# Kernel tuning notes

Measured on AMD Instinct MI355X. Metric: run time of the kernel, lower is better.

The kernel has to match this reference:

```python
import jax, jax.numpy as jnp
import numpy as np

D_MODEL = 1024
N_HEADS = 16
D_K = D_MODEL // N_HEADS
B, L = 4, 2048


def setup_inputs() -> dict:
    key = jax.random.key(0)
    ks = jax.random.split(key, 9)
    s = 1.0 / np.sqrt(D_MODEL)
    return {
        "x": jax.random.normal(ks[0], (B, L, D_MODEL), dtype=jnp.float32),
        "mask": jnp.ones((B, L), dtype=jnp.int32),
        "Wq": jax.random.uniform(ks[1], (D_MODEL, D_MODEL), jnp.float32, -s, s),
        "bq": jax.random.uniform(ks[2], (D_MODEL,), jnp.float32, -s, s),
        "Wk": jax.random.uniform(ks[3], (D_MODEL, D_MODEL), jnp.float32, -s, s),
        "bk": jax.random.uniform(ks[4], (D_MODEL,), jnp.float32, -s, s),
        "Wv": jax.random.uniform(ks[5], (D_MODEL, D_MODEL), jnp.float32, -s, s),
        "bv": jax.random.uniform(ks[6], (D_MODEL,), jnp.float32, -s, s),
        "Wo": jax.random.uniform(ks[7], (D_MODEL, D_MODEL), jnp.float32, -s, s),
        "bo": jax.random.uniform(ks[8], (D_MODEL,), jnp.float32, -s, s),
    }


def reference(x, mask, Wq, bq, Wk, bk, Wv, bv, Wo, bo):
    b, l, d = x.shape
    # project and split heads: [B, H, L, d_k]
    def heads(W, bias):
        return (x @ W.T + bias).reshape(b, l, N_HEADS, D_K).transpose(0, 2, 1, 3)
    Q = heads(Wq, bq)
    K = heads(Wk, bk)
    V = heads(Wv, bv)
    scores = jnp.einsum("bhqd,bhkd->bhqk", Q, K) / np.sqrt(D_K).astype(np.float32)
    # mask: [B, L] -> broadcast over heads and query dim as [B, 1, 1, L]
    scores = jnp.where(mask[:, None, None, :] == 0, jnp.float32(-1e9), scores)
    attn = jax.nn.softmax(scores, axis=-1)  # dropout=0 in eval math
    out = jnp.einsum("bhqk,bhkd->bhqd", attn, V)
    out = out.transpose(0, 2, 1, 3).reshape(b, l, d)
    return out @ Wo.T + bo
```

## Files before the change

### kernel.cpp

```cpp
#include <hip/hip_runtime.h>
#include <stdint.h>

#define DMODEL 1024
#define NHEADS 16
#define DK     64
#define BATCH  4
#define SEQ    2048
#define MROWS  (BATCH*SEQ)

typedef __bf16 bf16x8 __attribute__((ext_vector_type(8)));
typedef float  f32x4  __attribute__((ext_vector_type(4)));

#if defined(__has_builtin)
#if __has_builtin(__builtin_amdgcn_exp2f)
#define EXP2F(x) __builtin_amdgcn_exp2f(x)
#endif
#endif
#ifndef EXP2F
#define EXP2F(x) exp2f(x)
#endif

__device__ __forceinline__ unsigned short f2bf(float f) {
    unsigned int u = __builtin_bit_cast(unsigned int, f);
    u += 0x7fffu + ((u >> 16) & 1u);
    return (unsigned short)(u >> 16);
}

__device__ __forceinline__ unsigned int pack_bf16(float a, float b) {
    unsigned int ua = __builtin_bit_cast(unsigned int, a) + 0x8000u;
    unsigned int ub = __builtin_bit_cast(unsigned int, b) + 0x8000u;
    return __builtin_amdgcn_perm(ub, ua, 0x07060302u);
}

#define GLDS(gp, lp) __builtin_amdgcn_global_load_lds( \
    (const __attribute__((address_space(1))) unsigned int*)(gp), \
    (__attribute__((address_space(3))) unsigned int*)(lp), 16, 0, 0)

__global__ void cvt_kernel(const float* __restrict__ src,
                           unsigned short* __restrict__ dst, int n4) {
    int i = blockIdx.x * blockDim.x + threadIdx.x;
    if (i >= n4) return;
    const float4 v = reinterpret_cast<const float4*>(src)[i];
    ushort4 o;
    o.x = f2bf(v.x); o.y = f2bf(v.y); o.z = f2bf(v.z); o.w = f2bf(v.w);
    reinterpret_cast<ushort4*>(dst)[i] = o;
}

__global__ void cvtw_kernel(const float* __restrict__ w0, const float* __restrict__ w1,
                            const float* __restrict__ w2, const float* __restrict__ w3,
                            unsigned short* __restrict__ d0, unsigned short* __restrict__ d1,
                            unsigned short* __restrict__ d2, unsigned short* __restrict__ d3) {
    const float* s; unsigned short* d;
    switch (blockIdx.y) {
        case 0:  s = w0; d = d0; break;
        case 1:  s = w1; d = d1; break;
        case 2:  s = w2; d = d2; break;
        default: s = w3; d = d3; break;
    }
    const int i = blockIdx.x * blockDim.x + threadIdx.x;
    const float4 v = reinterpret_cast<const float4*>(s)[i];
    ushort4 o;
    o.x = f2bf(v.x); o.y = f2bf(v.y); o.z = f2bf(v.z); o.w = f2bf(v.w);
    reinterpret_cast<ushort4*>(d)[i] = o;
}

__global__ void maskbias_kernel(const int* __restrict__ m, float* __restrict__ o, int n) {
    const int i = blockIdx.x * blockDim.x + threadIdx.x;
    if (i < n) o[i] = m[i] ? 0.f : -1e30f;
}

template<int MODE>
__global__ __launch_bounds__(512, 1) void gemm256(
        const unsigned short* __restrict__ A,
        const unsigned short* __restrict__ W0,
        const unsigned short* __restrict__ W1,
        const unsigned short* __restrict__ W2,
        const float* __restrict__ b0,
        const float* __restrict__ b1,
        const float* __restrict__ b2,
        void* __restrict__ o0, void* __restrict__ o1, void* __restrict__ o2) {
    __shared__ unsigned short As[2][256 * 64];
    __shared__ unsigned short Bs[2][128 * 64];
    const int tid  = threadIdx.x;
    const int lane = tid & 63;
    const int wave = tid >> 6;
    const int quad = lane >> 4;
    const int r15  = lane & 15;
    const int wr = wave >> 1, wc = wave & 1;
    const int m0 = blockIdx.y * 256;

    int which, ncol0;
    const unsigned short* W;
    const float* bias;
    if (MODE == 0) {
        which = blockIdx.x >> 3;
        ncol0 = (blockIdx.x & 7) * 128;
        W    = which == 0 ? W0 : (which == 1 ? W1 : W2);
        bias = which == 0 ? b0 : (which == 1 ? b1 : b2);
    } else {
        which = 0; ncol0 = blockIdx.x * 128; W = W0; bias = b0;
    }

    const int srow = lane >> 3;
    const int scg  = (lane & 7) ^ srow;
    const unsigned short* Ag[4];
    const unsigned short* Wg[2];
    #pragma unroll
    for (int j = 0; j < 4; ++j)
        Ag[j] = A + (size_t)(m0 + j * 64 + wave * 8 + srow) * DMODEL + scg * 8;
    #pragma unroll
    for (int j = 0; j < 2; ++j)
        Wg[j] = W + (size_t)(ncol0 + j * 64 + wave * 8 + srow) * DMODEL + scg * 8;

    f32x4 acc[4][4] = {};

    #pragma unroll
    for (int j = 0; j < 4; ++j) GLDS(Ag[j], &As[0][(j * 64 + wave * 8) * 64]);
    #pragma unroll
    for (int j = 0; j < 2; ++j) GLDS(Wg[j], &Bs[0][(j * 64 + wave * 8) * 64]);
    __syncthreads();

    int buf = 0;
    for (int kk = 0; kk < DMODEL; kk += 64) {
        if (kk + 64 < DMODEL) {
            #pragma unroll
            for (int j = 0; j < 4; ++j)
                GLDS(Ag[j] + kk + 64, &As[buf ^ 1][(j * 64 + wave * 8) * 64]);
            #pragma unroll
            for (int j = 0; j < 2; ++j)
                GLDS(Wg[j] + kk + 64, &Bs[buf ^ 1][(j * 64 + wave * 8) * 64]);
        }
        #pragma unroll
        for (int u = 0; u < 2; ++u) {
            bf16x8 af[4], bfx[4];
            const int cs = ((u * 4 + quad) ^ (r15 & 7)) * 8;
            #pragma unroll
            for (int t = 0; t < 4; ++t) {
                af[t]  = *(const bf16x8*)&As[buf][(wr * 64 + t * 16 + r15) * 64 + cs];
                bfx[t] = *(const bf16x8*)&Bs[buf][(wc * 64 + t * 16 + r15) * 64 + cs];
            }
            #pragma unroll
            for (int mt = 0; mt < 4; ++mt)
                #pragma unroll
                for (int nt = 0; nt < 4; ++nt)
                    acc[mt][nt] = __builtin_amdgcn_mfma_f32_16x16x32_bf16(
                        af[mt], bfx[nt], acc[mt][nt], 0, 0, 0);
        }
        __syncthreads();
        buf ^= 1;
    }

    #pragma unroll
    for (int mt = 0; mt < 4; ++mt) {
        #pragma unroll
        for (int nt = 0; nt < 4; ++nt) {
            #pragma unroll
            for (int r = 0; r < 4; ++r) {
                const int row = m0 + wr * 64 + mt * 16 + quad * 4 + r;
                const int col = ncol0 + wc * 64 + nt * 16 + r15;
                float v = acc[mt][nt][r] + bias[col];
                if (MODE == 1) {
                    ((float*)o0)[(size_t)row * DMODEL + col] = v;
                } else {
                    if (which == 0) v *= 0.18033688011112042f;
                    const int b = row >> 11, l = row & (SEQ - 1);
                    const int h = col >> 6,  d = col & (DK - 1);
                    const int bh = b * NHEADS + h;
                    unsigned short* ow = (unsigned short*)(which == 0 ? o0 : (which == 1 ? o1 : o2));
                    size_t idx;
                    if (which < 2) idx = ((size_t)bh * SEQ + l) * DK + d;
                    else           idx = (size_t)bh * (SEQ * DK) + (l >> 6) * (DK * 64) + d * 64 + (l & 63);
                    ow[idx] = f2bf(v);
                }
            }
        }
    }
}

__global__ __launch_bounds__(256, 4) void flash_attn(
        const unsigned short* __restrict__ Q,
        const unsigned short* __restrict__ Km,
        const unsigned short* __restrict__ Vm,
        const float* __restrict__ mbf,
        unsigned short* __restrict__ Oa) {
    __shared__ unsigned short Ks[2][64 * 64];
    __shared__ unsigned short Vs[64 * 64];
    __shared__ unsigned short Pl[4][2][16 * 64];
    const int lane = threadIdx.x & 63;
    const int wave = threadIdx.x >> 6;
    const int quad = lane >> 4;
    const int r15  = lane & 15;

    const int id   = (blockIdx.y << 4) | blockIdx.x;
    const int xcd  = id & 7;
    const int slot = id >> 3;
    const int bh   = xcd + ((slot >> 4) << 3);
    const int qt   = slot & 15;
    const int b = bh >> 4, h = bh & (NHEADS - 1);
    const int q0 = qt * 128 + wave * 32;

    const unsigned short* Qb = Q  + (size_t)bh * SEQ * DK;
    const unsigned short* Kb = Km + (size_t)bh * SEQ * DK;
    const unsigned short* Vb = Vm + (size_t)bh * SEQ * DK;
    const float* mb = mbf + b * SEQ;

    const int srow = lane >> 3;
    const int soff = ((lane >> 3) * 64) + (((lane & 7) ^ srow) * 8);

    bf16x8 bq[2][2];
    #pragma unroll
    for (int qf = 0; qf < 2; ++qf)
        #pragma unroll
        for (int u = 0; u < 2; ++u)
            bq[qf][u] = *(const bf16x8*)(Qb + (q0 + qf * 16 + r15) * DK + u * 32 + quad * 8);

    float l_part[2] = {0.f, 0.f};
    f32x4 oacc[2][4] = {};

    #pragma unroll
    for (int j = 0; j < 2; ++j) {
        const int wseg = wave * 2 + j;
        GLDS(Kb + wseg * 512 + soff, &Ks[0][wseg * 512]);
        GLDS(Vb + wseg * 512 + soff, &Vs[wseg * 512]);
    }
    __syncthreads();

    #define NT (SEQ / 64)
    for (int t = 0; t < NT; ++t) {
        const int kb = t * 64;
        const int cur = t & 1;

        float4 m4v[4];
        #pragma unroll
        for (int tt = 0; tt < 4; ++tt)
            m4v[tt] = *(const float4*)(mb + kb + tt * 16 + quad * 4);

        if (t + 1 < NT) {
            const unsigned short* Kg = Kb + (kb + 64) * 64;
            #pragma unroll
            for (int j = 0; j < 2; ++j) {
                const int wseg = wave * 2 + j;
                GLDS(Kg + wseg * 512 + soff, &Ks[cur ^ 1][wseg * 512]);
            }
        }

        char* const Pb = (char*)&Pl[wave][0][0];
        #pragma unroll
        for (int tt = 0; tt < 4; ++tt) {
            const bf16x8 ak0 = *(const bf16x8*)&Ks[cur][(tt * 16 + r15) * 64 + ((quad ^ (r15 & 7)) * 8)];
            const bf16x8 ak1 = *(const bf16x8*)&Ks[cur][(tt * 16 + r15) * 64 + (((4 + quad) ^ (r15 & 7)) * 8)];
            const float4 m4 = m4v[tt];
            #pragma unroll
            for (int qf = 0; qf < 2; ++qf) {
                f32x4 z = {};
                z = __builtin_amdgcn_mfma_f32_16x16x32_bf16(ak0, bq[qf][0], z, 0, 0, 0);
                z = __builtin_amdgcn_mfma_f32_16x16x32_bf16(ak1, bq[qf][1], z, 0, 0, 0);
                const float p0 = EXP2F(z[0] + m4.x);
                const float p1 = EXP2F(z[1] + m4.y);
                const float p2 = EXP2F(z[2] + m4.z);
                const float p3 = EXP2F(z[3] + m4.w);
                l_part[qf] += (p0 + p1) + (p2 + p3);
                uint2 pw;
                pw.x = pack_bf16(p0, p1);
                pw.y = pack_bf16(p2, p3);
                const int c2 = (tt * 2 + (quad >> 1)) ^ (r15 & 7);
                *(uint2*)(Pb + qf * 2048 + r15 * 128 + c2 * 16 + (quad & 1) * 8) = pw;
            }
        }

        __syncthreads();

        __builtin_amdgcn_s_setprio(1);
        #pragma unroll
        for (int u = 0; u < 2; ++u) {
            const int cs = ((u * 4 + quad) ^ (r15 & 7)) * 8;
            bf16x8 vf[4];
            #pragma unroll
            for (int nt = 0; nt < 4; ++nt)
                vf[nt] = *(const bf16x8*)&Vs[(nt * 16 + r15) * 64 + cs];
            #pragma unroll
            for (int qf = 0; qf < 2; ++qf) {
                const bf16x8 ap = *(const bf16x8*)(Pb + qf * 2048 + r15 * 128 + cs * 2);
                #pragma unroll
                for (int nt = 0; nt < 4; ++nt)
                    oacc[qf][nt] = __builtin_amdgcn_mfma_f32_16x16x32_bf16(
                        ap, vf[nt], oacc[qf][nt], 0, 0, 0);
            }
        }
        __builtin_amdgcn_s_setprio(0);

        __syncthreads();

        if (t + 1 < NT) {
            const unsigned short* Vg = Vb + (kb + 64) * 64;
            #pragma unroll
            for (int j = 0; j < 2; ++j) {
                const int wseg = wave * 2 + j;
                GLDS(Vg + wseg * 512 + soff, &Vs[wseg * 512]);
            }
        }
    }
    #undef NT

    #pragma unroll
    for (int qf = 0; qf < 2; ++qf) {
        float l = l_part[qf];
        l += __shfl_xor(l, 16);
        l += __shfl_xor(l, 32);
        float lq[4];
        #pragma unroll
        for (int r = 0; r < 4; ++r) lq[r] = __shfl(l, quad * 4 + r, 64);
        #pragma unroll
        for (int nt = 0; nt < 4; ++nt) {
            #pragma unroll
            for (int r = 0; r < 4; ++r) {
                const int row = q0 + qf * 16 + quad * 4 + r;
                const int col = h * DK + nt * 16 + r15;
                Oa[((size_t)b * SEQ + row) * DMODEL + col] = f2bf(oacc[qf][nt][r] / lq[r]);
            }
        }
    }
}

extern "C" void kernel_launch(void* const* d_in, const int* in_sizes, int n_in,
                              void* d_out, int out_size, void* d_ws, size_t ws_size,
                              hipStream_t stream) {
    (void)in_sizes; (void)n_in; (void)out_size; (void)ws_size;
    const float* x  = (const float*)d_in[0];
    const int* mask = (const int*)d_in[1];
    const float* Wq = (const float*)d_in[2];
    const float* bq = (const float*)d_in[3];
    const float* Wk = (const float*)d_in[4];
    const float* bk = (const float*)d_in[5];
    const float* Wv = (const float*)d_in[6];
    const float* bv = (const float*)d_in[7];
    const float* Wo = (const float*)d_in[8];
    const float* bo = (const float*)d_in[9];
    float* out = (float*)d_out;

    char* ws = (char*)d_ws;
    unsigned short* xb  = (unsigned short*)(ws);
    unsigned short* wqb = (unsigned short*)(ws + 16777216);
    unsigned short* wkb = (unsigned short*)(ws + 16777216 + 1 * 2097152);
    unsigned short* wvb = (unsigned short*)(ws + 16777216 + 2 * 2097152);
    unsigned short* wob = (unsigned short*)(ws + 16777216 + 3 * 2097152);
    unsigned short* qb  = (unsigned short*)(ws + 16777216 + 4 * 2097152);
    unsigned short* kb  = qb  + (size_t)MROWS * DMODEL;
    unsigned short* vtb = kb  + (size_t)MROWS * DMODEL;
    unsigned short* ab  = vtb + (size_t)MROWS * DMODEL;
    float*          mbf = (float*)(ab + (size_t)MROWS * DMODEL);

    cvt_kernel<<<dim3(MROWS * DMODEL / 4 / 256), 256, 0, stream>>>(x, xb, MROWS * DMODEL / 4);
    cvtw_kernel<<<dim3(DMODEL * DMODEL / 4 / 256, 4), 256, 0, stream>>>(
        Wq, Wk, Wv, Wo, wqb, wkb, wvb, wob);
    maskbias_kernel<<<dim3(BATCH * SEQ / 256), 256, 0, stream>>>(mask, mbf, BATCH * SEQ);

    gemm256<0><<<dim3(24, MROWS / 256), 512, 0, stream>>>(
        xb, wqb, wkb, wvb, bq, bk, bv, qb, kb, vtb);

    flash_attn<<<dim3(16, BATCH * NHEADS), 256, 0, stream>>>(qb, kb, vtb, mbf, ab);

    gemm256<1><<<dim3(8, MROWS / 256), 512, 0, stream>>>(
        ab, wob, nullptr, nullptr, bo, nullptr, nullptr, out, nullptr, nullptr);
}
```

Before: 318.6 us.

## Triple-buffer GEMM LDS stages with split prefetch and raw barriers

Both GEMMs move from double to triple buffering of the A/W tiles in LDS. The loads for stage t+2 are issued in two halves interleaved with the two MFMA sub-steps. Full __syncthreads are replaced with raw s_barrier plus explicit vmcnt waits, and s_setprio is raised around the MFMA blocks. The aim is to hide global-to-LDS latency and cut barrier stalls, at the cost of about 1.5x the LDS (144KB) and hand-managed waitcnt counts that must stay correct.

```diff
diff --git a/kernel.cpp b/kernel.cpp
--- a/kernel.cpp
+++ b/kernel.cpp
@@ -35,6 +35,9 @@
 #define GLDS(gp, lp) __builtin_amdgcn_global_load_lds( \
     (const __attribute__((address_space(1))) unsigned int*)(gp), \
     (__attribute__((address_space(3))) unsigned int*)(lp), 16, 0, 0)
+
+#define RAW_BARRIER() do { asm volatile("" ::: "memory"); \
+    __builtin_amdgcn_s_barrier(); asm volatile("" ::: "memory"); } while (0)
 
 __global__ void cvt_kernel(const float* __restrict__ src,
                            unsigned short* __restrict__ dst, int n4) {
@@ -70,7 +73,7 @@
 }
 
 template<int MODE>
-__global__ __launch_bounds__(512, 1) void gemm256(
+__global__ __launch_bounds__(512, 1) void gemm8p(
         const unsigned short* __restrict__ A,
         const unsigned short* __restrict__ W0,
         const unsigned short* __restrict__ W1,
@@ -79,8 +82,8 @@
         const float* __restrict__ b1,
         const float* __restrict__ b2,
         void* __restrict__ o0, void* __restrict__ o1, void* __restrict__ o2) {
-    __shared__ unsigned short As[2][256 * 64];
-    __shared__ unsigned short Bs[2][128 * 64];
+    __shared__ unsigned short As[3][256 * 64];
+    __shared__ unsigned short Bs[3][128 * 64];
     const int tid  = threadIdx.x;
     const int lane = tid & 63;
     const int wave = tid >> 6;
@@ -111,43 +114,67 @@
     #pragma unroll
     for (int j = 0; j < 2; ++j)
         Wg[j] = W + (size_t)(ncol0 + j * 64 + wave * 8 + srow) * DMODEL + scg * 8;
+    const int lA = (wave * 8) * 64;
+    const int lB = (wave * 8) * 64;
 
     f32x4 acc[4][4] = {};
 
     #pragma unroll
-    for (int j = 0; j < 4; ++j) GLDS(Ag[j], &As[0][(j * 64 + wave * 8) * 64]);
-    #pragma unroll
-    for (int j = 0; j < 2; ++j) GLDS(Wg[j], &Bs[0][(j * 64 + wave * 8) * 64]);
-    __syncthreads();
-
-    int buf = 0;
-    for (int kk = 0; kk < DMODEL; kk += 64) {
-        if (kk + 64 < DMODEL) {
-            #pragma unroll
-            for (int j = 0; j < 4; ++j)
-                GLDS(Ag[j] + kk + 64, &As[buf ^ 1][(j * 64 + wave * 8) * 64]);
-            #pragma unroll
-            for (int j = 0; j < 2; ++j)
-                GLDS(Wg[j] + kk + 64, &Bs[buf ^ 1][(j * 64 + wave * 8) * 64]);
-        }
+    for (int j = 0; j < 4; ++j) GLDS(Ag[j],      &As[0][j * 4096 + lA]);
+    #pragma unroll
+    for (int j = 0; j < 2; ++j) GLDS(Wg[j],      &Bs[0][j * 4096 + lB]);
+    #pragma unroll
+    for (int j = 0; j < 4; ++j) GLDS(Ag[j] + 64, &As[1][j * 4096 + lA]);
+    #pragma unroll
+    for (int j = 0; j < 2; ++j) GLDS(Wg[j] + 64, &Bs[1][j * 4096 + lB]);
+    asm volatile("s_waitcnt vmcnt(6)" ::: "memory");
+    RAW_BARRIER();
+
+    const int NT = DMODEL / 64;
+    int rb = 0, sb = 2;
+    for (int t = 0; t < NT; ++t) {
+        const unsigned short* Asr = &As[rb][0];
+        const unsigned short* Bsr = &Bs[rb][0];
+        const int doStage = (t + 2 < NT);
+        const int koff = (t + 2) * 64;
+
         #pragma unroll
         for (int u = 0; u < 2; ++u) {
             bf16x8 af[4], bfx[4];
             const int cs = ((u * 4 + quad) ^ (r15 & 7)) * 8;
             #pragma unroll
-            for (int t = 0; t < 4; ++t) {
-                af[t]  = *(const bf16x8*)&As[buf][(wr * 64 + t * 16 + r15) * 64 + cs];
-                bfx[t] = *(const bf16x8*)&Bs[buf][(wc * 64 + t * 16 + r15) * 64 + cs];
-            }
+            for (int t4 = 0; t4 < 4; ++t4) {
+                af[t4]  = *(const bf16x8*)&Asr[(wr * 64 + t4 * 16 + r15) * 64 + cs];
+                bfx[t4] = *(const bf16x8*)&Bsr[(wc * 64 + t4 * 16 + r15) * 64 + cs];
+            }
+            if (doStage) {
+                if (u == 0) {
+                    GLDS(Ag[0] + koff, &As[sb][0 * 4096 + lA]);
+                    GLDS(Ag[1] + koff, &As[sb][1 * 4096 + lA]);
+                    GLDS(Wg[0] + koff, &Bs[sb][0 * 4096 + lB]);
+                } else {
+                    GLDS(Ag[2] + koff, &As[sb][2 * 4096 + lA]);
+                    GLDS(Ag[3] + koff, &As[sb][3 * 4096 + lA]);
+                    GLDS(Wg[1] + koff, &Bs[sb][1 * 4096 + lB]);
+                }
+            }
+            RAW_BARRIER();
+            __builtin_amdgcn_s_setprio(1);
             #pragma unroll
             for (int mt = 0; mt < 4; ++mt)
                 #pragma unroll
                 for (int nt = 0; nt < 4; ++nt)
                     acc[mt][nt] = __builtin_amdgcn_mfma_f32_16x16x32_bf16(
                         af[mt], bfx[nt], acc[mt][nt], 0, 0, 0);
-        }
-        __syncthreads();
-        buf ^= 1;
+            __builtin_amdgcn_s_setprio(0);
+            if (u == 1 && t + 1 < NT) {
+                if (doStage) asm volatile("s_waitcnt vmcnt(6)" ::: "memory");
+                else         asm volatile("s_waitcnt vmcnt(0)" ::: "memory");
+            }
+            RAW_BARRIER();
+        }
+        rb = (rb == 2) ? 0 : rb + 1;
+        sb = (sb == 2) ? 0 : sb + 1;
     }
 
     #pragma unroll
@@ -355,11 +382,11 @@
         Wq, Wk, Wv, Wo, wqb, wkb, wvb, wob);
     maskbias_kernel<<<dim3(BATCH * SEQ / 256), 256, 0, stream>>>(mask, mbf, BATCH * SEQ);
 
-    gemm256<0><<<dim3(24, MROWS / 256), 512, 0, stream>>>(
+    gemm8p<0><<<dim3(24, MROWS / 256), 512, 0, stream>>>(
         xb, wqb, wkb, wvb, bq, bk, bv, qb, kb, vtb);
 
     flash_attn<<<dim3(16, BATCH * NHEADS), 256, 0, stream>>>(qb, kb, vtb, mbf, ab);
 
-    gemm256<1><<<dim3(8, MROWS / 256), 512, 0, stream>>>(
+    gemm8p<1><<<dim3(8, MROWS / 256), 512, 0, stream>>>(
         ab, wob, nullptr, nullptr, bo, nullptr, nullptr, out, nullptr, nullptr);
 }
```

After: 320.7 us. Within noise of the previous version (+0.7%).
